# Performance work log

Measured on AMD Instinct MI355X. Metric: run time of the kernel, lower is better.

Reference implementation:

```python
import jax, jax.numpy as jnp
import numpy as np

B, C, F, N = 2, 8, 80, 128
H, W = 512, 1024


def setup_inputs() -> dict:
    key = jax.random.key(0)
    k1, k2, k3 = jax.random.split(key, 3)
    x = jax.random.normal(k1, (B, C, F, N, N), dtype=jnp.float32)
    quad = jax.random.randint(k2, (H, W), 0, F, dtype=jnp.int32)
    # uv buffer holds coordinates already scaled into [0, N-1]
    uv = jax.random.uniform(k3, (H, W, 2), dtype=jnp.float32) * (N - 1)
    return {"x": x, "quad": quad, "uv": uv}


def reference(x, quad, uv):
    """x: B x C x F x N x N texture patches; quad: H x W face indices;
    uv: H x W x 2 in-patch coordinates in [0, N-1]. Returns B x C x H x W."""
    Bx, Cx, Fx, Nx, _ = x.shape
    Hh, Ww = quad.shape
    u = uv[..., 0].reshape(-1)  # HW
    v = uv[..., 1].reshape(-1)
    u0 = jnp.clip(jnp.floor(u), 0, Nx - 2).astype(jnp.int32)
    v0 = jnp.clip(jnp.floor(v), 0, Nx - 2).astype(jnp.int32)
    du = u - u0.astype(u.dtype)
    dv = v - v0.astype(v.dtype)
    base = quad.reshape(-1).astype(jnp.int32) * (Nx * Nx)  # HW
    x_flat = x.reshape(Bx, Cx, Fx * Nx * Nx)
    i00 = base + v0 * Nx + u0
    g00 = x_flat[:, :, i00]           # B x C x HW
    g01 = x_flat[:, :, i00 + 1]
    g10 = x_flat[:, :, i00 + Nx]
    g11 = x_flat[:, :, i00 + Nx + 1]
    w00 = (1.0 - du) * (1.0 - dv)
    w01 = du * (1.0 - dv)
    w10 = (1.0 - du) * dv
    w11 = du * dv
    out = g00 * w00 + g01 * w01 + g10 * w10 + g11 * w11  # B x C x HW
    return out.reshape(Bx, Cx, Hh, Ww)
```

## Files before the change

kernel.cpp:

```cpp
#include <hip/hip_runtime.h>
#include <hip/hip_fp16.h>

#define BC   16
#define FD   80
#define ND   128
#define NN   (ND * ND)
#define HW   (512 * 1024)
#define HW_SHIFT 19

#define YH_BYTES ((size_t)FD * NN * BC * sizeof(__half))

typedef float  vf4 __attribute__((ext_vector_type(4)));
typedef float  vf2 __attribute__((ext_vector_type(2)));

__global__ __launch_bounds__(256)
void repack_kernel(const float* __restrict__ x, __half* __restrict__ y)
{
    const int tid = threadIdx.x;
    const int u2  = tid & 63;
    const int r   = tid >> 6;
    const int fv  = blockIdx.x * 4 + r;
    const int f   = fv >> 7;
    const int v   = fv & (ND - 1);

    const float* xp = x + ((size_t)f * ND + v) * ND + u2 * 2;
    vf2 g[BC];
#pragma unroll
    for (int c = 0; c < BC; ++c)
        g[c] = __builtin_nontemporal_load((const vf2*)(xp + (size_t)c * FD * NN));

    uint4 oo[4];
    unsigned* w = (unsigned*)oo;
#pragma unroll
    for (int j = 0; j < 4; ++j) {
        const __half2 h0 = __floats2half2_rn(g[2 * j].x,     g[2 * j + 1].x);
        const __half2 h1 = __floats2half2_rn(g[8 + 2 * j].x, g[9 + 2 * j].x);
        const __half2 h2 = __floats2half2_rn(g[2 * j].y,     g[2 * j + 1].y);
        const __half2 h3 = __floats2half2_rn(g[8 + 2 * j].y, g[9 + 2 * j].y);
        w[j]      = *(const unsigned*)&h0;
        w[4 + j]  = *(const unsigned*)&h1;
        w[8 + j]  = *(const unsigned*)&h2;
        w[12 + j] = *(const unsigned*)&h3;
    }

    uint4* dst = (uint4*)(y + ((size_t)fv * ND + u2 * 2) * BC);
#pragma unroll
    for (int k = 0; k < 4; ++k) dst[k] = oo[k];
}

__device__ inline void acc8p(float2* o2, uint4 t, float w)
{
    const unsigned* p = (const unsigned*)&t;
#pragma unroll
    for (int j = 0; j < 4; ++j) {
        const float2 fp = __half22float2(*(const __half2*)&p[j]);
        o2[j].x += fp.x * w;
        o2[j].y += fp.y * w;
    }
}

__global__ __launch_bounds__(256)
void gather_kernel(const __half* __restrict__ y,
                   const int*    __restrict__ quad,
                   const float2* __restrict__ uv2,
                   float* __restrict__ out)
{
    const int pix = blockIdx.x * 256 + threadIdx.x;

    const vf2 tv = __builtin_nontemporal_load((const vf2*)&uv2[pix]);
    const int f  = __builtin_nontemporal_load(&quad[pix]);

    const float u = tv.x;
    const float v = tv.y;

    int u0 = (int)floorf(u);
    int v0 = (int)floorf(v);
    u0 = min(max(u0, 0), ND - 2);
    v0 = min(max(v0, 0), ND - 2);

    const size_t base = (((size_t)f * ND + v0) * ND + u0) * BC;
    const uint4* r0 = (const uint4*)(y + base);
    const uint4* r1 = (const uint4*)(y + base + (size_t)ND * BC);
    const uint4 a0 = r0[0], a1 = r0[1];
    const uint4 b0 = r0[2], b1 = r0[3];
    const uint4 c0 = r1[0], c1 = r1[1];
    const uint4 d0 = r1[2], d1 = r1[3];

    const float du = u - (float)u0;
    const float dv = v - (float)v0;
    const float w00 = (1.0f - du) * (1.0f - dv);
    const float w01 = du * (1.0f - dv);
    const float w10 = (1.0f - du) * dv;
    const float w11 = du * dv;

    float2 o2[8];
#pragma unroll
    for (int j = 0; j < 8; ++j) o2[j] = make_float2(0.0f, 0.0f);

    acc8p(o2,     a0, w00); acc8p(o2 + 4, a1, w00);
    acc8p(o2,     b0, w01); acc8p(o2 + 4, b1, w01);
    acc8p(o2,     c0, w10); acc8p(o2 + 4, c1, w10);
    acc8p(o2,     d0, w11); acc8p(o2 + 4, d1, w11);

    const float* o = (const float*)o2;
#pragma unroll
    for (int c = 0; c < BC; ++c)
        __builtin_nontemporal_store(o[c], &out[(size_t)c * HW + pix]);
}

__global__ __launch_bounds__(256)
void resample_fallback_kernel(const float* __restrict__ x,
                              const int*   __restrict__ quad,
                              const float2* __restrict__ uv2,
                              float* __restrict__ out)
{
    const int gid = blockIdx.x * 256 + threadIdx.x;
    const int pix = gid & (HW - 1);
    const int bc  = gid >> HW_SHIFT;

    const float2 t = uv2[pix];
    const int    f = quad[pix];

    const float u = t.x;
    const float v = t.y;

    int u0 = (int)floorf(u);
    int v0 = (int)floorf(v);
    u0 = min(max(u0, 0), ND - 2);
    v0 = min(max(v0, 0), ND - 2);

    const float du = u - (float)u0;
    const float dv = v - (float)v0;

    const float w00 = (1.0f - du) * (1.0f - dv);
    const float w01 = du * (1.0f - dv);
    const float w10 = (1.0f - du) * dv;
    const float w11 = du * dv;

    const float* p = x + ((size_t)bc * FD + (size_t)f) * NN + v0 * ND + u0;
    out[gid] = p[0] * w00 + p[1] * w01 + p[ND] * w10 + p[ND + 1] * w11;
}

extern "C" void kernel_launch(void* const* d_in, const int* in_sizes, int n_in,
                              void* d_out, int out_size, void* d_ws, size_t ws_size,
                              hipStream_t stream)
{
    const float*  x    = (const float*)d_in[0];
    const int*    quad = (const int*)d_in[1];
    const float2* uv2  = (const float2*)d_in[2];
    float*        out  = (float*)d_out;

    if (ws_size >= YH_BYTES) {
        __half* y = (__half*)d_ws;
        repack_kernel<<<FD * ND / 4, 256, 0, stream>>>(x, y);
        gather_kernel<<<HW / 256, 256, 0, stream>>>(y, quad, uv2, out);
    } else {
        const int total = BC * HW;
        resample_fallback_kernel<<<total / 256, 256, 0, stream>>>(x, quad, uv2, out);
    }
}
```

Baseline: 165.6 us.

## Repack texels with duplicated right neighbour and gather two pixels per thread

The repack now writes each texel entry as 32 halfs: the texel's 16 channels followed by its right neighbour's 16 channels. A bilinear tap pair then comes from one contiguous 64-byte segment, so each row's two corners share cache lines. The gather kernel handles two pixels per thread with vectorized uv/quad loads and float2 output stores. The cost is a workspace twice as large, so the repack writes twice the bytes, and a shuffle is needed at row boundaries. If the workspace is too small, the fallback kernel runs instead.

```diff
diff --git a/kernel.cpp b/kernel.cpp
--- a/kernel.cpp
+++ b/kernel.cpp
@@ -8,44 +8,58 @@
 #define HW   (512 * 1024)
 #define HW_SHIFT 19
 
-#define YH_BYTES ((size_t)FD * NN * BC * sizeof(__half))
+#define YH2_BYTES ((size_t)FD * ND * ND * 64)
 
-typedef float  vf4 __attribute__((ext_vector_type(4)));
-typedef float  vf2 __attribute__((ext_vector_type(2)));
+typedef float vf4 __attribute__((ext_vector_type(4)));
+typedef float vf2 __attribute__((ext_vector_type(2)));
+typedef int   vi2 __attribute__((ext_vector_type(2)));
 
 __global__ __launch_bounds__(256)
 void repack_kernel(const float* __restrict__ x, __half* __restrict__ y)
 {
     const int tid = threadIdx.x;
-    const int u2  = tid & 63;
-    const int r   = tid >> 6;
-    const int fv  = blockIdx.x * 4 + r;
+    const int q   = tid & 31;
+    const int r   = tid >> 5;
+    const int fv  = blockIdx.x * 8 + r;
     const int f   = fv >> 7;
     const int v   = fv & (ND - 1);
 
-    const float* xp = x + ((size_t)f * ND + v) * ND + u2 * 2;
-    vf2 g[BC];
+    const float* xp = x + ((size_t)f * ND + v) * ND + q * 4;
+    vf4 g[BC];
 #pragma unroll
     for (int c = 0; c < BC; ++c)
-        g[c] = __builtin_nontemporal_load((const vf2*)(xp + (size_t)c * FD * NN));
+        g[c] = __builtin_nontemporal_load((const vf4*)(xp + (size_t)c * FD * NN));
 
-    uint4 oo[4];
-    unsigned* w = (unsigned*)oo;
+    float xn[BC];
 #pragma unroll
-    for (int j = 0; j < 4; ++j) {
-        const __half2 h0 = __floats2half2_rn(g[2 * j].x,     g[2 * j + 1].x);
-        const __half2 h1 = __floats2half2_rn(g[8 + 2 * j].x, g[9 + 2 * j].x);
-        const __half2 h2 = __floats2half2_rn(g[2 * j].y,     g[2 * j + 1].y);
-        const __half2 h3 = __floats2half2_rn(g[8 + 2 * j].y, g[9 + 2 * j].y);
-        w[j]      = *(const unsigned*)&h0;
-        w[4 + j]  = *(const unsigned*)&h1;
-        w[8 + j]  = *(const unsigned*)&h2;
-        w[12 + j] = *(const unsigned*)&h3;
+    for (int c = 0; c < BC; ++c) {
+        const float s = __shfl_down(g[c].x, 1);
+        xn[c] = (q == 31) ? g[c].w : s;
     }
 
-    uint4* dst = (uint4*)(y + ((size_t)fv * ND + u2 * 2) * BC);
+    unsigned Ad[4][8], Bd[8];
 #pragma unroll
-    for (int k = 0; k < 4; ++k) dst[k] = oo[k];
+    for (int e = 0; e < 4; ++e)
+#pragma unroll
+        for (int j = 0; j < 8; ++j) {
+            const __half2 h = __floats2half2_rn(g[2 * j][e], g[2 * j + 1][e]);
+            Ad[e][j] = *(const unsigned*)&h;
+        }
+#pragma unroll
+    for (int j = 0; j < 8; ++j) {
+        const __half2 h = __floats2half2_rn(xn[2 * j], xn[2 * j + 1]);
+        Bd[j] = *(const unsigned*)&h;
+    }
+
+    uint4* dst = (uint4*)(y + ((size_t)fv * ND + q * 4) * 32);
+#pragma unroll
+    for (int e = 0; e < 4; ++e) {
+        const unsigned* Bp = (e < 3) ? Ad[e + 1] : Bd;
+        dst[e * 4 + 0] = make_uint4(Ad[e][0], Ad[e][1], Ad[e][2], Ad[e][3]);
+        dst[e * 4 + 1] = make_uint4(Ad[e][4], Ad[e][5], Ad[e][6], Ad[e][7]);
+        dst[e * 4 + 2] = make_uint4(Bp[0], Bp[1], Bp[2], Bp[3]);
+        dst[e * 4 + 3] = make_uint4(Bp[4], Bp[5], Bp[6], Bp[7]);
+    }
 }
 
 __device__ inline void acc8p(float2* o2, uint4 t, float w)
@@ -59,28 +73,17 @@
     }
 }
 
-__global__ __launch_bounds__(256)
-void gather_kernel(const __half* __restrict__ y,
-                   const int*    __restrict__ quad,
-                   const float2* __restrict__ uv2,
-                   float* __restrict__ out)
+__device__ inline void gather_one(const __half* __restrict__ y,
+                                  float u, float v, int f, float2* o2)
 {
-    const int pix = blockIdx.x * 256 + threadIdx.x;
-
-    const vf2 tv = __builtin_nontemporal_load((const vf2*)&uv2[pix]);
-    const int f  = __builtin_nontemporal_load(&quad[pix]);
-
-    const float u = tv.x;
-    const float v = tv.y;
-
     int u0 = (int)floorf(u);
     int v0 = (int)floorf(v);
     u0 = min(max(u0, 0), ND - 2);
     v0 = min(max(v0, 0), ND - 2);
 
-    const size_t base = (((size_t)f * ND + v0) * ND + u0) * BC;
-    const uint4* r0 = (const uint4*)(y + base);
-    const uint4* r1 = (const uint4*)(y + base + (size_t)ND * BC);
+    const size_t entry = ((size_t)f * ND + v0) * ND + u0;
+    const uint4* r0 = (const uint4*)(y + entry * 32);
+    const uint4* r1 = r0 + 512;
     const uint4 a0 = r0[0], a1 = r0[1];
     const uint4 b0 = r0[2], b1 = r0[3];
     const uint4 c0 = r1[0], c1 = r1[1];
@@ -93,19 +96,41 @@
     const float w10 = (1.0f - du) * dv;
     const float w11 = du * dv;
 
-    float2 o2[8];
-#pragma unroll
-    for (int j = 0; j < 8; ++j) o2[j] = make_float2(0.0f, 0.0f);
-
     acc8p(o2,     a0, w00); acc8p(o2 + 4, a1, w00);
     acc8p(o2,     b0, w01); acc8p(o2 + 4, b1, w01);
     acc8p(o2,     c0, w10); acc8p(o2 + 4, c1, w10);
     acc8p(o2,     d0, w11); acc8p(o2 + 4, d1, w11);
+}
 
-    const float* o = (const float*)o2;
+__global__ __launch_bounds__(256)
+void gather_kernel(const __half* __restrict__ y,
+                   const int*    __restrict__ quad,
+                   const float2* __restrict__ uv2,
+                   float* __restrict__ out)
+{
+    const int gid  = blockIdx.x * 256 + threadIdx.x;
+    const int pix0 = gid * 2;
+
+    const vf4 tv = __builtin_nontemporal_load((const vf4*)&uv2[pix0]);
+    const vi2 ff = __builtin_nontemporal_load((const vi2*)&quad[pix0]);
+
+    float2 oA[8], oB[8];
 #pragma unroll
-    for (int c = 0; c < BC; ++c)
-        __builtin_nontemporal_store(o[c], &out[(size_t)c * HW + pix]);
+    for (int j = 0; j < 8; ++j) {
+        oA[j] = make_float2(0.0f, 0.0f);
+        oB[j] = make_float2(0.0f, 0.0f);
+    }
+
+    gather_one(y, tv.x, tv.y, ff.x, oA);
+    gather_one(y, tv.z, tv.w, ff.y, oB);
+
+    const float* a = (const float*)oA;
+    const float* b = (const float*)oB;
+#pragma unroll
+    for (int c = 0; c < BC; ++c) {
+        vf2 s; s.x = a[c]; s.y = b[c];
+        __builtin_nontemporal_store(s, (vf2*)&out[(size_t)c * HW + pix0]);
+    }
 }
 
 __global__ __launch_bounds__(256)
@@ -150,10 +175,10 @@
     const float2* uv2  = (const float2*)d_in[2];
     float*        out  = (float*)d_out;
 
-    if (ws_size >= YH_BYTES) {
+    if (ws_size >= YH2_BYTES) {
         __half* y = (__half*)d_ws;
-        repack_kernel<<<FD * ND / 4, 256, 0, stream>>>(x, y);
-        gather_kernel<<<HW / 256, 256, 0, stream>>>(y, quad, uv2, out);
+        repack_kernel<<<FD * ND / 8, 256, 0, stream>>>(x, y);
+        gather_kernel<<<HW / 512, 256, 0, stream>>>(y, quad, uv2, out);
     } else {
         const int total = BC * HW;
         resample_fallback_kernel<<<total / 256, 256, 0, stream>>>(x, quad, uv2, out);
```

Result: slower. 184.6 us (+11.5%).
